# Kernel optimization log

Hardware: AMD Instinct MI355X
Metric: run time of the kernel (lower is better)

Reference implementation:

```python
import jax, jax.numpy as jnp
import numpy as np

# irreps_in == irreps_out == 512x0e + 256x1o + 128x2e
# each entry: (multiplicity, irrep dimension 2l+1)
IRREPS = [(512, 1), (256, 3), (128, 5)]
DIM_TOTAL = sum(m * d for m, d in IRREPS)          # 1920
WEIGHT_NUMEL = sum(m * m for m, _ in IRREPS)       # 344064
N = 16384


def setup_inputs() -> dict:
    key = jax.random.key(0)
    kx, kw = jax.random.split(key)
    x = jax.random.normal(kx, (N, DIM_TOTAL), dtype=jnp.float32)
    weight = jax.random.normal(kw, (WEIGHT_NUMEL,), dtype=jnp.float32)
    return {"x": x, "weight": weight}


def reference(x, weight):
    """Segmented (block-diagonal per irrep) linear mixing with 1/sqrt(fan_in) norm."""
    n = x.shape[0]
    outs = []
    x_off = 0
    w_off = 0
    for mul, d in IRREPS:
        seg = x[:, x_off:x_off + mul * d].reshape(n, mul, d)      # [N, mul, 2l+1]
        W = weight[w_off:w_off + mul * mul].reshape(mul, mul)     # [mul_in, mul_out]
        scale = jnp.asarray(1.0 / np.sqrt(mul), dtype=x.dtype)
        y = jnp.einsum('nui,uv->nvi', seg, W) * scale             # channel mix per component
        outs.append(y.reshape(n, mul * d))
        x_off += mul * d
        w_off += mul * mul
    return jnp.concatenate(outs, axis=-1)
```

## Files before the change

### kernel.cpp

```cpp
#include <hip/hip_runtime.h>


typedef float  f32x4  __attribute__((ext_vector_type(4)));
typedef short  bf16x8 __attribute__((ext_vector_type(8)));

#define ROWLEN 1920

__device__ __forceinline__ unsigned short f2bf(float f) {
    union { float f; unsigned int u; } c; c.f = f;
    unsigned int u = c.u;
    u += 0x7fffu + ((u >> 16) & 1u);
    return (unsigned short)(u >> 16);
}

__global__ __launch_bounds__(256) void prep_weights(const float* __restrict__ w,
                                                    unsigned short* __restrict__ wt) {
    const int g = blockIdx.x * 256 + threadIdx.x;
    if (g >= 344064) return;
    int base, lmul;
    if      (g < 262144) { base = 0;      lmul = 9; }
    else if (g < 327680) { base = 262144; lmul = 8; }
    else                 { base = 327680; lmul = 7; }
    const int local = g - base;
    const int u = local >> lmul;
    const int v = local & ((1 << lmul) - 1);
    const int nstep_log = lmul - 5;
    const int vt   = v >> 4;
    const int ks   = u >> 5;
    const int lane = (((u >> 3) & 3) << 4) | (v & 15);
    const int j    = u & 7;
    wt[base + ((((vt << nstep_log) + ks) << 6) + lane) * 8 + j] = f2bf(w[g]);
}

template<int MUL, int D, int TN, int X_OFF, int WT_BASE>
__device__ __forceinline__ void seg_body(const int bid,
                                         const float* __restrict__ x,
                                         const unsigned short* __restrict__ wt,
                                         float* __restrict__ out,
                                         const float scale,
                                         unsigned short* lds) {
    constexpr int KB      = 32;
    constexpr int NSTEP   = MUL / KB;
    constexpr int M_LOG   = TN * D;
    constexpr int MT      = M_LOG / 16;
    constexpr int NWAVE   = 8;
    constexpr int WAVE_NT = MUL / (NWAVE * 16);
    constexpr int ST      = MUL + 8;
    constexpr int ROW_F4  = MUL * D / 4;
    constexpr int ITERS   = TN * ROW_F4 / (NWAVE * 64);
    constexpr int TVS     = NSTEP * 512;
    constexpr bool BREG   = (WAVE_NT * NSTEP) <= 16;

    const int tid  = threadIdx.x;
    const int wave = tid >> 6;
    const int lane = tid & 63;
    const int q    = lane >> 4;
    const int t16  = lane & 15;
    const int n0   = bid * TN;

    const float* __restrict__ xblk = x + X_OFF + n0 * ROWLEN;
    const unsigned short* __restrict__ wfrag =
        wt + WT_BASE + (wave * WAVE_NT) * TVS + lane * 8;

    f32x4 acc[MT][WAVE_NT];
#pragma unroll
    for (int a = 0; a < MT; ++a)
#pragma unroll
        for (int b = 0; b < WAVE_NT; ++b) acc[a][b] = (f32x4)0.0f;

    auto stage_tile = [&]() {
#pragma unroll
        for (int it = 0; it < ITERS; ++it) {
            const int idx = tid + it * (NWAVE * 64);
            const int nl  = idx / ROW_F4;
            const int c4  = (idx - nl * ROW_F4) * 4;
            const f32x4 vv = *(const f32x4*)(xblk + nl * ROWLEN + c4);
            if (D == 1) {
                unsigned int lo = (unsigned int)f2bf(vv[0]) | ((unsigned int)f2bf(vv[1]) << 16);
                unsigned int hi = (unsigned int)f2bf(vv[2]) | ((unsigned int)f2bf(vv[3]) << 16);
                unsigned int* p = (unsigned int*)&lds[nl * ST + c4];
                p[0] = lo; p[1] = hi;
            } else {
#pragma unroll
                for (int e = 0; e < 4; ++e) {
                    const int c = c4 + e;
                    const int u = c / D;
                    const int i = c - u * D;
                    lds[(i * TN + nl) * ST + u] = f2bf(vv[e]);
                }
            }
        }
    };

    if constexpr (BREG) {
        bf16x8 breg[WAVE_NT * NSTEP];
#pragma unroll
        for (int tv = 0; tv < WAVE_NT; ++tv)
#pragma unroll
            for (int ks = 0; ks < NSTEP; ++ks)
                breg[tv * NSTEP + ks] = *(const bf16x8*)&wfrag[tv * TVS + ks * 512];
        stage_tile();
        __syncthreads();
#pragma unroll
        for (int ks = 0; ks < NSTEP; ++ks) {
            bf16x8 afr[MT];
#pragma unroll
            for (int tm = 0; tm < MT; ++tm)
                afr[tm] = *(const bf16x8*)&lds[(16 * tm + t16) * ST + ks * KB + q * 8];
#pragma unroll
            for (int tv = 0; tv < WAVE_NT; ++tv)
#pragma unroll
                for (int tm = 0; tm < MT; ++tm)
                    acc[tm][tv] = __builtin_amdgcn_mfma_f32_16x16x32_bf16(afr[tm], breg[tv * NSTEP + ks], acc[tm][tv], 0, 0, 0);
        }
    } else {
        constexpr int PF = 3;
        bf16x8 bfr[4][WAVE_NT];
#pragma unroll
        for (int p = 0; p < PF; ++p)
#pragma unroll
            for (int tv = 0; tv < WAVE_NT; ++tv)
                bfr[p][tv] = *(const bf16x8*)&wfrag[tv * TVS + p * 512];
        stage_tile();
        __syncthreads();
#pragma unroll
        for (int ks = 0; ks < NSTEP; ++ks) {
            if (ks + PF < NSTEP) {
#pragma unroll
                for (int tv = 0; tv < WAVE_NT; ++tv)
                    bfr[(ks + PF) & 3][tv] = *(const bf16x8*)&wfrag[tv * TVS + (ks + PF) * 512];
            }
            bf16x8 afr[MT];
#pragma unroll
            for (int tm = 0; tm < MT; ++tm)
                afr[tm] = *(const bf16x8*)&lds[(16 * tm + t16) * ST + ks * KB + q * 8];
#pragma unroll
            for (int tv = 0; tv < WAVE_NT; ++tv)
#pragma unroll
                for (int tm = 0; tm < MT; ++tm)
                    acc[tm][tv] = __builtin_amdgcn_mfma_f32_16x16x32_bf16(afr[tm], bfr[ks & 3][tv], acc[tm][tv], 0, 0, 0);
        }
    }

#pragma unroll
    for (int tm = 0; tm < MT; ++tm) {
#pragma unroll
        for (int tv = 0; tv < WAVE_NT; ++tv) {
            const int v = wave * (WAVE_NT * 16) + t16 + tv * 16;
#pragma unroll
            for (int r = 0; r < 4; ++r) {
                const int rit  = q * 4 + r;
                const int lrow = 16 * tm + rit;
                const int i    = lrow / TN;
                const int nl   = lrow - i * TN;
                out[(n0 + nl) * ROWLEN + X_OFF + v * D + i] = acc[tm][tv][r] * scale;
            }
        }
    }
}

__global__ __launch_bounds__(512, 4) void fused_gemm(const float* __restrict__ x,
                                                     const unsigned short* __restrict__ wt,
                                                     float* __restrict__ out) {
    extern __shared__ unsigned short lds[];
    const int b = blockIdx.x;
    const int g = b / 5;
    const int r = b - g * 5;
    if (r == 0) {
        seg_body<512, 1, 32, 0, 0>(g, x, wt, out, 0.044194173824f, lds);
    } else if (r <= 2) {
        seg_body<256, 3, 16, 512, 262144>(g * 2 + (r - 1), x, wt, out, 0.0625f, lds);
    } else {
        seg_body<128, 5, 16, 1280, 327680>(g * 2 + (r - 3), x, wt, out, 0.088388347648f, lds);
    }
}

extern "C" void kernel_launch(void* const* d_in, const int* in_sizes, int n_in,
                              void* d_out, int out_size, void* d_ws, size_t ws_size,
                              hipStream_t stream) {
    const float* x = (const float*)d_in[0];
    const float* w = (const float*)d_in[1];
    float* out = (float*)d_out;
    unsigned short* wt = (unsigned short*)d_ws;

    hipLaunchKernelGGL(prep_weights, dim3(1344), dim3(256), 0, stream, w, wt);
    hipLaunchKernelGGL(fused_gemm, dim3(2560), dim3(512), 33280, stream, x, wt, out);
}
```

Before: 235.8 us.

## Double row tile per block and simplify weight fragment prefetch to two stages

Each segment block now handles twice as many rows (64/32/32), so grid size halves and dynamic LDS doubles to 66560 bytes. Every weight fragment loaded from global memory is therefore reused across twice as many rows, which cuts weight traffic. The register-resident weight path and the 3-deep prefetch are replaced by one 2-stage double-buffered prefetch, and weight loads now start after the x tile is staged rather than overlapping with it. In exchange, the larger LDS footprint and more accumulator registers (MT doubles) may lower occupancy, and there are fewer blocks to spread across CUs.

```diff
diff --git a/kernel.cpp b/kernel.cpp
--- a/kernel.cpp
+++ b/kernel.cpp
@@ -43,13 +43,11 @@
     constexpr int NSTEP   = MUL / KB;
     constexpr int M_LOG   = TN * D;
     constexpr int MT      = M_LOG / 16;
-    constexpr int NWAVE   = 8;
-    constexpr int WAVE_NT = MUL / (NWAVE * 16);
+    constexpr int WAVE_NT = MUL / 128;
     constexpr int ST      = MUL + 8;
     constexpr int ROW_F4  = MUL * D / 4;
-    constexpr int ITERS   = TN * ROW_F4 / (NWAVE * 64);
+    constexpr int ITERS   = TN * ROW_F4 / 512;
     constexpr int TVS     = NSTEP * 512;
-    constexpr bool BREG   = (WAVE_NT * NSTEP) <= 16;
 
     const int tid  = threadIdx.x;
     const int wave = tid >> 6;
@@ -68,77 +66,52 @@
 #pragma unroll
         for (int b = 0; b < WAVE_NT; ++b) acc[a][b] = (f32x4)0.0f;
 
-    auto stage_tile = [&]() {
 #pragma unroll
-        for (int it = 0; it < ITERS; ++it) {
-            const int idx = tid + it * (NWAVE * 64);
-            const int nl  = idx / ROW_F4;
-            const int c4  = (idx - nl * ROW_F4) * 4;
-            const f32x4 vv = *(const f32x4*)(xblk + nl * ROWLEN + c4);
-            if (D == 1) {
-                unsigned int lo = (unsigned int)f2bf(vv[0]) | ((unsigned int)f2bf(vv[1]) << 16);
-                unsigned int hi = (unsigned int)f2bf(vv[2]) | ((unsigned int)f2bf(vv[3]) << 16);
-                unsigned int* p = (unsigned int*)&lds[nl * ST + c4];
-                p[0] = lo; p[1] = hi;
-            } else {
+    for (int it = 0; it < ITERS; ++it) {
+        const int idx = tid + it * 512;
+        const int nl  = idx / ROW_F4;
+        const int c4  = (idx - nl * ROW_F4) * 4;
+        const f32x4 vv = *(const f32x4*)(xblk + nl * ROWLEN + c4);
+        if (D == 1) {
+            unsigned int lo = (unsigned int)f2bf(vv[0]) | ((unsigned int)f2bf(vv[1]) << 16);
+            unsigned int hi = (unsigned int)f2bf(vv[2]) | ((unsigned int)f2bf(vv[3]) << 16);
+            unsigned int* p = (unsigned int*)&lds[nl * ST + c4];
+            p[0] = lo; p[1] = hi;
+        } else {
 #pragma unroll
-                for (int e = 0; e < 4; ++e) {
-                    const int c = c4 + e;
-                    const int u = c / D;
-                    const int i = c - u * D;
-                    lds[(i * TN + nl) * ST + u] = f2bf(vv[e]);
-                }
+            for (int e = 0; e < 4; ++e) {
+                const int c = c4 + e;
+                const int u = c / D;
+                const int i = c - u * D;
+                lds[(i * TN + nl) * ST + u] = f2bf(vv[e]);
             }
         }
-    };
+    }
 
-    if constexpr (BREG) {
-        bf16x8 breg[WAVE_NT * NSTEP];
+    __syncthreads();
+
+    bf16x8 bfr[2][WAVE_NT];
+#pragma unroll
+    for (int p = 0; p < 2; ++p)
+#pragma unroll
+        for (int tv = 0; tv < WAVE_NT; ++tv)
+            bfr[p][tv] = *(const bf16x8*)&wfrag[tv * TVS + p * 512];
+
+#pragma unroll
+    for (int ks = 0; ks < NSTEP; ++ks) {
+        bf16x8 afr[MT];
+#pragma unroll
+        for (int tm = 0; tm < MT; ++tm)
+            afr[tm] = *(const bf16x8*)&lds[(16 * tm + t16) * ST + ks * KB + q * 8];
 #pragma unroll
         for (int tv = 0; tv < WAVE_NT; ++tv)
 #pragma unroll
-            for (int ks = 0; ks < NSTEP; ++ks)
-                breg[tv * NSTEP + ks] = *(const bf16x8*)&wfrag[tv * TVS + ks * 512];
-        stage_tile();
-        __syncthreads();
-#pragma unroll
-        for (int ks = 0; ks < NSTEP; ++ks) {
-            bf16x8 afr[MT];
-#pragma unroll
             for (int tm = 0; tm < MT; ++tm)
-                afr[tm] = *(const bf16x8*)&lds[(16 * tm + t16) * ST + ks * KB + q * 8];
+                acc[tm][tv] = __builtin_amdgcn_mfma_f32_16x16x32_bf16(afr[tm], bfr[ks & 1][tv], acc[tm][tv], 0, 0, 0);
+        if (ks + 2 < NSTEP) {
 #pragma unroll
             for (int tv = 0; tv < WAVE_NT; ++tv)
-#pragma unroll
-                for (int tm = 0; tm < MT; ++tm)
-                    acc[tm][tv] = __builtin_amdgcn_mfma_f32_16x16x32_bf16(afr[tm], breg[tv * NSTEP + ks], acc[tm][tv], 0, 0, 0);
-        }
-    } else {
-        constexpr int PF = 3;
-        bf16x8 bfr[4][WAVE_NT];
-#pragma unroll
-        for (int p = 0; p < PF; ++p)
-#pragma unroll
-            for (int tv = 0; tv < WAVE_NT; ++tv)
-                bfr[p][tv] = *(const bf16x8*)&wfrag[tv * TVS + p * 512];
-        stage_tile();
-        __syncthreads();
-#pragma unroll
-        for (int ks = 0; ks < NSTEP; ++ks) {
-            if (ks + PF < NSTEP) {
-#pragma unroll
-                for (int tv = 0; tv < WAVE_NT; ++tv)
-                    bfr[(ks + PF) & 3][tv] = *(const bf16x8*)&wfrag[tv * TVS + (ks + PF) * 512];
-            }
-            bf16x8 afr[MT];
-#pragma unroll
-            for (int tm = 0; tm < MT; ++tm)
-                afr[tm] = *(const bf16x8*)&lds[(16 * tm + t16) * ST + ks * KB + q * 8];
-#pragma unroll
-            for (int tv = 0; tv < WAVE_NT; ++tv)
-#pragma unroll
-                for (int tm = 0; tm < MT; ++tm)
-                    acc[tm][tv] = __builtin_amdgcn_mfma_f32_16x16x32_bf16(afr[tm], bfr[ks & 3][tv], acc[tm][tv], 0, 0, 0);
+                bfr[ks & 1][tv] = *(const bf16x8*)&wfrag[tv * TVS + (ks + 2) * 512];
         }
     }
 
@@ -167,11 +140,11 @@
     const int g = b / 5;
     const int r = b - g * 5;
     if (r == 0) {
-        seg_body<512, 1, 32, 0, 0>(g, x, wt, out, 0.044194173824f, lds);
+        seg_body<512, 1, 64, 0, 0>(g, x, wt, out, 0.044194173824f, lds);
     } else if (r <= 2) {
-        seg_body<256, 3, 16, 512, 262144>(g * 2 + (r - 1), x, wt, out, 0.0625f, lds);
+        seg_body<256, 3, 32, 512, 262144>(g * 2 + (r - 1), x, wt, out, 0.0625f, lds);
     } else {
-        seg_body<128, 5, 16, 1280, 327680>(g * 2 + (r - 3), x, wt, out, 0.088388347648f, lds);
+        seg_body<128, 5, 32, 1280, 327680>(g * 2 + (r - 3), x, wt, out, 0.088388347648f, lds);
     }
 }
 
@@ -184,5 +157,5 @@
     unsigned short* wt = (unsigned short*)d_ws;
 
     hipLaunchKernelGGL(prep_weights, dim3(1344), dim3(256), 0, stream, w, wt);
-    hipLaunchKernelGGL(fused_gemm, dim3(2560), dim3(512), 33280, stream, x, wt, out);
+    hipLaunchKernelGGL(fused_gemm, dim3(1280), dim3(512), 66560, stream, x, wt, out);
 }
```

Measured after the change: 272.0 us. 1.15x slower.
